# Kernel tuning notes

Measured on AMD Instinct MI355X. Metric: run time of the kernel, lower is better.

## Reference

```python
import jax, jax.numpy as jnp
import numpy as np

N_NODES = 100000
N_EDGES = 3200000


def gcn_conv(x, row, col, W, n):
    # PyG GCNConv: x @ W, then D^{-1/2}(A+I)D^{-1/2} aggregation (self-loops added).
    h = x @ W  # [N, out]
    loop = jnp.arange(n)
    r = jnp.concatenate([row, loop])
    c = jnp.concatenate([col, loop])
    deg = jax.ops.segment_sum(jnp.ones_like(c, dtype=h.dtype), c, num_segments=n)
    dinv = jnp.where(deg > 0, jax.lax.rsqrt(deg), 0.0)
    norm = dinv[r] * dinv[c]  # [E+N]
    msg = h[r] * norm[:, None]  # gather + scale
    return jax.ops.segment_sum(msg, c, num_segments=n)  # scatter-add


def setup_inputs() -> dict:
    key = jax.random.key(0)
    k1, k2, k3, k4, k5 = jax.random.split(key, 5)
    x = jax.random.normal(k1, (N_NODES, 1), dtype=jnp.float32)
    edge_index = jax.random.randint(k2, (2, N_EDGES), 0, N_NODES, dtype=jnp.int64)
    W1 = jax.random.normal(k3, (1, 16), dtype=jnp.float32) * 0.5
    W2 = jax.random.normal(k4, (16, 16), dtype=jnp.float32) * 0.25
    W3 = jax.random.normal(k5, (16, 11), dtype=jnp.float32) * 0.25
    b = jnp.zeros((11,), dtype=jnp.float32)
    return {"x": x, "edge_index": edge_index, "W1": W1, "W2": W2, "W3": W3, "b": b}


def reference(x, edge_index, W1, W2, W3, b):
    n = x.shape[0]
    row, col = edge_index[0], edge_index[1]
    h = jax.nn.relu(gcn_conv(x, row, col, W1, n))
    h = jax.nn.relu(gcn_conv(h, row, col, W2, n))
    g = jnp.mean(h, axis=0).reshape(-1, 16)  # [1,16] graph readout
    out = (g @ W3).squeeze() + b  # [11]
    return out
```

## Files before the change

kernel.cpp:

```cpp
#include <hip/hip_runtime.h>

static constexpr int N = 100000;
static constexpr int E = 3200000;
static constexpr int BUKSHIFT = 8;
static constexpr int BUKSZ = 1 << BUKSHIFT;
static constexpr int BUKMASK = BUKSZ - 1;
static constexpr int NBUK = (N + BUKSZ - 1) / BUKSZ;
static constexpr int CAP = 12288;
static constexpr int SC_CHUNK = 8192;
static constexpr int SC_T = 1024;
static constexpr int SC_BLOCKS = (E + SC_CHUNK - 1) / SC_CHUNK;


__global__ void k_init(int* __restrict__ gofs) {
    int i = threadIdx.x;
    if (i < NBUK) gofs[i] = i * CAP;
}

__global__ __launch_bounds__(SC_T) void k_scatter(const int4* __restrict__ rows4,
                                                  const int4* __restrict__ cols4,
                                                  int* __restrict__ gofs,
                                                  int* __restrict__ binned) {
    __shared__ int hist[4][NBUK];
    __shared__ int cnt[512];
    __shared__ int lbase[NBUK];
    __shared__ int gbase[NBUK];
    __shared__ int stag[SC_CHUNK];

    const int tid = threadIdx.x;
    const int g = tid >> 8;
    for (int i = tid; i < 4 * NBUK; i += SC_T) (&hist[0][0])[i] = 0;
    if (tid < 512) cnt[tid] = 0;
    __syncthreads();

    const int nI4 = E / 4;
    const int base4 = blockIdx.x * (SC_CHUNK / 4);
    const int ia = base4 + tid, ib = base4 + 1024 + tid;
    const bool va = ia < nI4, vb = ib < nI4;
    int4 ra, ca, rb, cb;
    if (va) { ra = rows4[ia]; ca = cols4[ia]; }
    if (vb) { rb = rows4[ib]; cb = cols4[ib]; }

    if (va) {
        atomicAdd(&hist[g][ca.x >> BUKSHIFT], 1);
        atomicAdd(&hist[g][ca.y >> BUKSHIFT], 1);
        atomicAdd(&hist[g][ca.z >> BUKSHIFT], 1);
        atomicAdd(&hist[g][ca.w >> BUKSHIFT], 1);
    }
    if (vb) {
        atomicAdd(&hist[g][cb.x >> BUKSHIFT], 1);
        atomicAdd(&hist[g][cb.y >> BUKSHIFT], 1);
        atomicAdd(&hist[g][cb.z >> BUKSHIFT], 1);
        atomicAdd(&hist[g][cb.w >> BUKSHIFT], 1);
    }
    __syncthreads();

    if (tid < NBUK) {
        int h0 = hist[0][tid], h1 = hist[1][tid], h2 = hist[2][tid], h3 = hist[3][tid];
        hist[0][tid] = 0; hist[1][tid] = h0; hist[2][tid] = h0 + h1; hist[3][tid] = h0 + h1 + h2;
        int c = h0 + h1 + h2 + h3;
        cnt[tid] = c;
        gbase[tid] = c ? atomicAdd(&gofs[tid], c) : 0;
    }
    __syncthreads();
    for (int off = 1; off < 512; off <<= 1) {
        int v = 0;
        if (tid < 512) { v = cnt[tid]; if (tid >= off) v += cnt[tid - off]; }
        __syncthreads();
        if (tid < 512) cnt[tid] = v;
        __syncthreads();
    }
    if (tid < NBUK) lbase[tid] = tid ? cnt[tid - 1] : 0;
    __syncthreads();

    if (va) {
        int b, off;
        b = ca.x >> BUKSHIFT; off = atomicAdd(&hist[g][b], 1); stag[lbase[b] + off] = (ra.x << BUKSHIFT) | (ca.x & BUKMASK);
        b = ca.y >> BUKSHIFT; off = atomicAdd(&hist[g][b], 1); stag[lbase[b] + off] = (ra.y << BUKSHIFT) | (ca.y & BUKMASK);
        b = ca.z >> BUKSHIFT; off = atomicAdd(&hist[g][b], 1); stag[lbase[b] + off] = (ra.z << BUKSHIFT) | (ca.z & BUKMASK);
        b = ca.w >> BUKSHIFT; off = atomicAdd(&hist[g][b], 1); stag[lbase[b] + off] = (ra.w << BUKSHIFT) | (ca.w & BUKMASK);
    }
    if (vb) {
        int b, off;
        b = cb.x >> BUKSHIFT; off = atomicAdd(&hist[g][b], 1); stag[lbase[b] + off] = (rb.x << BUKSHIFT) | (cb.x & BUKMASK);
        b = cb.y >> BUKSHIFT; off = atomicAdd(&hist[g][b], 1); stag[lbase[b] + off] = (rb.y << BUKSHIFT) | (cb.y & BUKMASK);
        b = cb.z >> BUKSHIFT; off = atomicAdd(&hist[g][b], 1); stag[lbase[b] + off] = (rb.z << BUKSHIFT) | (cb.z & BUKMASK);
        b = cb.w >> BUKSHIFT; off = atomicAdd(&hist[g][b], 1); stag[lbase[b] + off] = (rb.w << BUKSHIFT) | (cb.w & BUKMASK);
    }
    __syncthreads();

    const int eTot = min(SC_CHUNK, E - blockIdx.x * SC_CHUNK);
    int s = tid * 8;
    if (s < eTot) {
        int lo = 0, hi = NBUK - 1;
        while (lo < hi) { int mid = (lo + hi + 1) >> 1; if (lbase[mid] <= s) lo = mid; else hi = mid - 1; }
        int b = lo;
        const int e1 = min(s + 8, eTot);
        for (; s < e1; ++s) {
            while (b + 1 < NBUK && lbase[b + 1] <= s) ++b;
            binned[gbase[b] + (s - lbase[b])] = stag[s];
        }
    }
}

__global__ void k_deg(const int* __restrict__ binned, const int* __restrict__ gofs,
                      const float* __restrict__ x, float* __restrict__ dinv,
                      float* __restrict__ y1) {
    __shared__ int cnt[2][BUKSZ];
    const int tid = threadIdx.x;
    cnt[0][tid] = 0; cnt[1][tid] = 0;
    __syncthreads();
    const int b = blockIdx.x, g = tid >> 7;
    const int s1 = gofs[b];
    for (int i = b * CAP + tid; i < s1; i += 256)
        atomicAdd(&cnt[g][binned[i] & BUKMASK], 1);
    __syncthreads();
    const int v = (b << BUKSHIFT) + tid;
    if (v < N) {
        float d = rsqrtf(1.0f + (float)(cnt[0][tid] + cnt[1][tid]));
        dinv[v] = d;
        y1[v] = d * x[v];
    }
}

__global__ void k_acc1(const int* __restrict__ binned, const int* __restrict__ gofs,
                       const float* __restrict__ y1, const float* __restrict__ dinv,
                       float* __restrict__ m) {
    __shared__ float acc[2][BUKSZ];
    const int tid = threadIdx.x;
    acc[0][tid] = 0.f; acc[1][tid] = 0.f;
    __syncthreads();
    const int b = blockIdx.x, g = tid >> 7;
    const int s1 = gofs[b];
    for (int i = b * CAP + tid; i < s1; i += 256) {
        int p = binned[i];
        atomicAdd(&acc[g][p & BUKMASK], y1[p >> BUKSHIFT]);
    }
    __syncthreads();
    const int v = (b << BUKSHIFT) + tid;
    if (v < N) {
        float d = dinv[v];
        float s = d * (acc[0][tid] + acc[1][tid]) + d * y1[v];
        m[v] = d * s;
    }
}

__global__ void k_acc2(const int* __restrict__ binned, const int* __restrict__ gofs,
                       const float* __restrict__ m, const float* __restrict__ dinv,
                       const float* __restrict__ W1, const float* __restrict__ W2,
                       float* __restrict__ partials) {
    __shared__ float tp[2][BUKSZ], tn[2][BUKSZ];
    __shared__ float sP[16], sM[16], sAcc[16];
    const int tid = threadIdx.x;
    if (tid < 16) {
        float p = 0.f, q = 0.f;
        for (int k = 0; k < 16; ++k) {
            float w1 = W1[k];
            float w2 = W2[k * 16 + tid];
            p += fmaxf(w1, 0.f) * w2;
            q += fminf(w1, 0.f) * w2;
        }
        sP[tid] = p; sM[tid] = q; sAcc[tid] = 0.f;
    }
    tp[0][tid] = 0.f; tp[1][tid] = 0.f; tn[0][tid] = 0.f; tn[1][tid] = 0.f;
    __syncthreads();
    const int b = blockIdx.x, g = tid >> 7;
    const int s1 = gofs[b];
    for (int i = b * CAP + tid; i < s1; i += 256) {
        int p = binned[i];
        float val = m[p >> BUKSHIFT];
        atomicAdd(val >= 0.f ? &tp[g][p & BUKMASK] : &tn[g][p & BUKMASK], val);
    }
    __syncthreads();
    const int v = (b << BUKSHIFT) + tid;
    float alpha = 0.f, beta = 0.f;
    if (v < N) {
        float d = dinv[v], mv = m[v];
        alpha = d * (tp[0][tid] + tp[1][tid]);
        beta  = d * (tn[0][tid] + tn[1][tid]);
        float self = d * mv;
        if (mv >= 0.f) alpha += self; else beta += self;
    }
    const int lane = tid & 63;
    for (int j = 0; j < 16; ++j) {
        float h = fmaxf(alpha * sP[j] + beta * sM[j], 0.f);
        #pragma unroll
        for (int off = 32; off > 0; off >>= 1) h += __shfl_down(h, off);
        if (lane == 0) atomicAdd(&sAcc[j], h);
    }
    __syncthreads();
    if (tid < 16) partials[b * 16 + tid] = sAcc[tid];
}

__global__ void k_out(const float* __restrict__ partials, const float* __restrict__ W3,
                      const float* __restrict__ b, float* __restrict__ out) {
    __shared__ float s[16][16];
    int j = threadIdx.x & 15;
    int g = threadIdx.x >> 4;
    float acc = 0.f;
    for (int blk = g; blk < NBUK; blk += 16) acc += partials[blk * 16 + j];
    s[g][j] = acc;
    __syncthreads();
    if (threadIdx.x < 16) {
        float tot = 0.f;
        #pragma unroll
        for (int gg = 0; gg < 16; ++gg) tot += s[gg][threadIdx.x];
        s[0][threadIdx.x] = tot * (1.0f / (float)N);
    }
    __syncthreads();
    if (threadIdx.x < 11) {
        float acc2 = b[threadIdx.x];
        #pragma unroll
        for (int k = 0; k < 16; ++k) acc2 += s[0][k] * W3[k * 11 + threadIdx.x];
        out[threadIdx.x] = acc2;
    }
}

extern "C" void kernel_launch(void* const* d_in, const int* in_sizes, int n_in,
                              void* d_out, int out_size, void* d_ws, size_t ws_size,
                              hipStream_t stream) {
    const float* x  = (const float*)d_in[0];
    const int*   ei = (const int*)d_in[1];
    const float* W1 = (const float*)d_in[2];
    const float* W2 = (const float*)d_in[3];
    const float* W3 = (const float*)d_in[4];
    const float* b  = (const float*)d_in[5];
    float* out = (float*)d_out;

    int*   wsi      = (int*)d_ws;
    int*   binned   = wsi;
    float* dinv     = (float*)(wsi + (size_t)NBUK * CAP);
    float* y1       = dinv + N;
    float* m        = y1 + N;
    int*   gofs     = (int*)(m + N);
    float* partials = (float*)(gofs + NBUK);

    const int4* rows4 = (const int4*)ei;
    const int4* cols4 = (const int4*)(ei + E);

    k_init   <<<1, 512, 0, stream>>>(gofs);
    k_scatter<<<SC_BLOCKS, SC_T, 0, stream>>>(rows4, cols4, gofs, binned);
    k_deg    <<<NBUK, 256, 0, stream>>>(binned, gofs, x, dinv, y1);
    k_acc1   <<<NBUK, 256, 0, stream>>>(binned, gofs, y1, dinv, m);
    k_acc2   <<<NBUK, 256, 0, stream>>>(binned, gofs, m, dinv, W1, W2, partials);
    k_out    <<<1, 256, 0, stream>>>(partials, W3, b, out);
}
```

Before: 104.8 us.

## Widen bucket kernels to 1024 threads with int4 loads and larger scatter chunks

The degree and both aggregation kernels now run 1024 threads per bucket. Each kernel reads the binned edge list as int4 and spreads its shared-memory atomics over 8 privatized histogram copies, which are summed at the end. The scatter kernel now handles 16384 edges per block, with each thread loading four int4 vectors. The goal is more memory-level parallelism and less contention on shared-memory atomics. The cost is half as many scatter blocks, which may leave CUs idle, and a larger shared-memory footprint per block.

```diff
diff --git a/kernel.cpp b/kernel.cpp
--- a/kernel.cpp
+++ b/kernel.cpp
@@ -7,7 +7,7 @@
 static constexpr int BUKMASK = BUKSZ - 1;
 static constexpr int NBUK = (N + BUKSZ - 1) / BUKSZ;
 static constexpr int CAP = 12288;
-static constexpr int SC_CHUNK = 8192;
+static constexpr int SC_CHUNK = 16384;
 static constexpr int SC_T = 1024;
 static constexpr int SC_BLOCKS = (E + SC_CHUNK - 1) / SC_CHUNK;
 
@@ -35,32 +35,29 @@
 
     const int nI4 = E / 4;
     const int base4 = blockIdx.x * (SC_CHUNK / 4);
-    const int ia = base4 + tid, ib = base4 + 1024 + tid;
-    const bool va = ia < nI4, vb = ib < nI4;
-    int4 ra, ca, rb, cb;
-    if (va) { ra = rows4[ia]; ca = cols4[ia]; }
-    if (vb) { rb = rows4[ib]; cb = cols4[ib]; }
-
-    if (va) {
-        atomicAdd(&hist[g][ca.x >> BUKSHIFT], 1);
-        atomicAdd(&hist[g][ca.y >> BUKSHIFT], 1);
-        atomicAdd(&hist[g][ca.z >> BUKSHIFT], 1);
-        atomicAdd(&hist[g][ca.w >> BUKSHIFT], 1);
-    }
-    if (vb) {
-        atomicAdd(&hist[g][cb.x >> BUKSHIFT], 1);
-        atomicAdd(&hist[g][cb.y >> BUKSHIFT], 1);
-        atomicAdd(&hist[g][cb.z >> BUKSHIFT], 1);
-        atomicAdd(&hist[g][cb.w >> BUKSHIFT], 1);
+    int4 r[4], c[4];
+    bool vld[4];
+    #pragma unroll
+    for (int k = 0; k < 4; ++k) {
+        int idx = base4 + k * SC_T + tid;
+        vld[k] = idx < nI4;
+        if (vld[k]) { r[k] = rows4[idx]; c[k] = cols4[idx]; }
+    }
+    #pragma unroll
+    for (int k = 0; k < 4; ++k) if (vld[k]) {
+        atomicAdd(&hist[g][c[k].x >> BUKSHIFT], 1);
+        atomicAdd(&hist[g][c[k].y >> BUKSHIFT], 1);
+        atomicAdd(&hist[g][c[k].z >> BUKSHIFT], 1);
+        atomicAdd(&hist[g][c[k].w >> BUKSHIFT], 1);
     }
     __syncthreads();
 
     if (tid < NBUK) {
         int h0 = hist[0][tid], h1 = hist[1][tid], h2 = hist[2][tid], h3 = hist[3][tid];
         hist[0][tid] = 0; hist[1][tid] = h0; hist[2][tid] = h0 + h1; hist[3][tid] = h0 + h1 + h2;
-        int c = h0 + h1 + h2 + h3;
-        cnt[tid] = c;
-        gbase[tid] = c ? atomicAdd(&gofs[tid], c) : 0;
+        int cc = h0 + h1 + h2 + h3;
+        cnt[tid] = cc;
+        gbase[tid] = cc ? atomicAdd(&gofs[tid], cc) : 0;
     }
     __syncthreads();
     for (int off = 1; off < 512; off <<= 1) {
@@ -73,29 +70,23 @@
     if (tid < NBUK) lbase[tid] = tid ? cnt[tid - 1] : 0;
     __syncthreads();
 
-    if (va) {
+    #pragma unroll
+    for (int k = 0; k < 4; ++k) if (vld[k]) {
         int b, off;
-        b = ca.x >> BUKSHIFT; off = atomicAdd(&hist[g][b], 1); stag[lbase[b] + off] = (ra.x << BUKSHIFT) | (ca.x & BUKMASK);
-        b = ca.y >> BUKSHIFT; off = atomicAdd(&hist[g][b], 1); stag[lbase[b] + off] = (ra.y << BUKSHIFT) | (ca.y & BUKMASK);
-        b = ca.z >> BUKSHIFT; off = atomicAdd(&hist[g][b], 1); stag[lbase[b] + off] = (ra.z << BUKSHIFT) | (ca.z & BUKMASK);
-        b = ca.w >> BUKSHIFT; off = atomicAdd(&hist[g][b], 1); stag[lbase[b] + off] = (ra.w << BUKSHIFT) | (ca.w & BUKMASK);
-    }
-    if (vb) {
-        int b, off;
-        b = cb.x >> BUKSHIFT; off = atomicAdd(&hist[g][b], 1); stag[lbase[b] + off] = (rb.x << BUKSHIFT) | (cb.x & BUKMASK);
-        b = cb.y >> BUKSHIFT; off = atomicAdd(&hist[g][b], 1); stag[lbase[b] + off] = (rb.y << BUKSHIFT) | (cb.y & BUKMASK);
-        b = cb.z >> BUKSHIFT; off = atomicAdd(&hist[g][b], 1); stag[lbase[b] + off] = (rb.z << BUKSHIFT) | (cb.z & BUKMASK);
-        b = cb.w >> BUKSHIFT; off = atomicAdd(&hist[g][b], 1); stag[lbase[b] + off] = (rb.w << BUKSHIFT) | (cb.w & BUKMASK);
+        b = c[k].x >> BUKSHIFT; off = atomicAdd(&hist[g][b], 1); stag[lbase[b] + off] = (r[k].x << BUKSHIFT) | (c[k].x & BUKMASK);
+        b = c[k].y >> BUKSHIFT; off = atomicAdd(&hist[g][b], 1); stag[lbase[b] + off] = (r[k].y << BUKSHIFT) | (c[k].y & BUKMASK);
+        b = c[k].z >> BUKSHIFT; off = atomicAdd(&hist[g][b], 1); stag[lbase[b] + off] = (r[k].z << BUKSHIFT) | (c[k].z & BUKMASK);
+        b = c[k].w >> BUKSHIFT; off = atomicAdd(&hist[g][b], 1); stag[lbase[b] + off] = (r[k].w << BUKSHIFT) | (c[k].w & BUKMASK);
     }
     __syncthreads();
 
     const int eTot = min(SC_CHUNK, E - blockIdx.x * SC_CHUNK);
-    int s = tid * 8;
+    int s = tid * 16;
     if (s < eTot) {
         int lo = 0, hi = NBUK - 1;
         while (lo < hi) { int mid = (lo + hi + 1) >> 1; if (lbase[mid] <= s) lo = mid; else hi = mid - 1; }
         int b = lo;
-        const int e1 = min(s + 8, eTot);
+        const int e1 = min(s + 16, eTot);
         for (; s < e1; ++s) {
             while (b + 1 < NBUK && lbase[b + 1] <= s) ++b;
             binned[gbase[b] + (s - lbase[b])] = stag[s];
@@ -103,53 +94,89 @@
     }
 }
 
-__global__ void k_deg(const int* __restrict__ binned, const int* __restrict__ gofs,
-                      const float* __restrict__ x, float* __restrict__ dinv,
-                      float* __restrict__ y1) {
-    __shared__ int cnt[2][BUKSZ];
-    const int tid = threadIdx.x;
-    cnt[0][tid] = 0; cnt[1][tid] = 0;
+__global__ __launch_bounds__(1024) void k_deg(const int* __restrict__ binned,
+                                              const int* __restrict__ gofs,
+                                              const float* __restrict__ x,
+                                              float* __restrict__ dinv,
+                                              float* __restrict__ y1) {
+    __shared__ int cnt[8][BUKSZ];
+    const int tid = threadIdx.x;
+    for (int i = tid; i < 8 * BUKSZ; i += 1024) (&cnt[0][0])[i] = 0;
     __syncthreads();
     const int b = blockIdx.x, g = tid >> 7;
-    const int s1 = gofs[b];
-    for (int i = b * CAP + tid; i < s1; i += 256)
-        atomicAdd(&cnt[g][binned[i] & BUKMASK], 1);
-    __syncthreads();
-    const int v = (b << BUKSHIFT) + tid;
-    if (v < N) {
-        float d = rsqrtf(1.0f + (float)(cnt[0][tid] + cnt[1][tid]));
-        dinv[v] = d;
-        y1[v] = d * x[v];
-    }
-}
-
-__global__ void k_acc1(const int* __restrict__ binned, const int* __restrict__ gofs,
-                       const float* __restrict__ y1, const float* __restrict__ dinv,
-                       float* __restrict__ m) {
-    __shared__ float acc[2][BUKSZ];
-    const int tid = threadIdx.x;
-    acc[0][tid] = 0.f; acc[1][tid] = 0.f;
+    const int s0 = b * CAP;
+    const int n = gofs[b] - s0;
+    const int n4 = n >> 2;
+    const int4* b4 = (const int4*)(binned + s0);
+    for (int i = tid; i < n4; i += 1024) {
+        int4 p = b4[i];
+        atomicAdd(&cnt[g][p.x & BUKMASK], 1);
+        atomicAdd(&cnt[g][p.y & BUKMASK], 1);
+        atomicAdd(&cnt[g][p.z & BUKMASK], 1);
+        atomicAdd(&cnt[g][p.w & BUKMASK], 1);
+    }
+    if (tid < (n & 3)) atomicAdd(&cnt[g][binned[s0 + (n4 << 2) + tid] & BUKMASK], 1);
+    __syncthreads();
+    if (tid < BUKSZ) {
+        int v = (b << BUKSHIFT) + tid;
+        if (v < N) {
+            int c = 0;
+            #pragma unroll
+            for (int q = 0; q < 8; ++q) c += cnt[q][tid];
+            float d = rsqrtf(1.0f + (float)c);
+            dinv[v] = d;
+            y1[v] = d * x[v];
+        }
+    }
+}
+
+__global__ __launch_bounds__(1024) void k_acc1(const int* __restrict__ binned,
+                                               const int* __restrict__ gofs,
+                                               const float* __restrict__ y1,
+                                               const float* __restrict__ dinv,
+                                               float* __restrict__ m) {
+    __shared__ float acc[8][BUKSZ];
+    const int tid = threadIdx.x;
+    for (int i = tid; i < 8 * BUKSZ; i += 1024) (&acc[0][0])[i] = 0.f;
     __syncthreads();
     const int b = blockIdx.x, g = tid >> 7;
-    const int s1 = gofs[b];
-    for (int i = b * CAP + tid; i < s1; i += 256) {
-        int p = binned[i];
+    const int s0 = b * CAP;
+    const int n = gofs[b] - s0;
+    const int n4 = n >> 2;
+    const int4* b4 = (const int4*)(binned + s0);
+    for (int i = tid; i < n4; i += 1024) {
+        int4 p = b4[i];
+        atomicAdd(&acc[g][p.x & BUKMASK], y1[p.x >> BUKSHIFT]);
+        atomicAdd(&acc[g][p.y & BUKMASK], y1[p.y >> BUKSHIFT]);
+        atomicAdd(&acc[g][p.z & BUKMASK], y1[p.z >> BUKSHIFT]);
+        atomicAdd(&acc[g][p.w & BUKMASK], y1[p.w >> BUKSHIFT]);
+    }
+    if (tid < (n & 3)) {
+        int p = binned[s0 + (n4 << 2) + tid];
         atomicAdd(&acc[g][p & BUKMASK], y1[p >> BUKSHIFT]);
     }
     __syncthreads();
-    const int v = (b << BUKSHIFT) + tid;
-    if (v < N) {
-        float d = dinv[v];
-        float s = d * (acc[0][tid] + acc[1][tid]) + d * y1[v];
-        m[v] = d * s;
-    }
-}
-
-__global__ void k_acc2(const int* __restrict__ binned, const int* __restrict__ gofs,
-                       const float* __restrict__ m, const float* __restrict__ dinv,
-                       const float* __restrict__ W1, const float* __restrict__ W2,
-                       float* __restrict__ partials) {
-    __shared__ float tp[2][BUKSZ], tn[2][BUKSZ];
+    if (tid < BUKSZ) {
+        int v = (b << BUKSHIFT) + tid;
+        if (v < N) {
+            float a = 0.f;
+            #pragma unroll
+            for (int q = 0; q < 8; ++q) a += acc[q][tid];
+            float d = dinv[v];
+            float s = d * a + d * y1[v];
+            m[v] = d * s;
+        }
+    }
+}
+
+__global__ __launch_bounds__(1024) void k_acc2(const int* __restrict__ binned,
+                                               const int* __restrict__ gofs,
+                                               const float* __restrict__ m,
+                                               const float* __restrict__ dinv,
+                                               const float* __restrict__ W1,
+                                               const float* __restrict__ W2,
+                                               float* __restrict__ partials) {
+    __shared__ float tp[8][BUKSZ], tn[8][BUKSZ];
     __shared__ float sP[16], sM[16], sAcc[16];
     const int tid = threadIdx.x;
     if (tid < 16) {
@@ -162,31 +189,48 @@
         }
         sP[tid] = p; sM[tid] = q; sAcc[tid] = 0.f;
     }
-    tp[0][tid] = 0.f; tp[1][tid] = 0.f; tn[0][tid] = 0.f; tn[1][tid] = 0.f;
+    for (int i = tid; i < 8 * BUKSZ; i += 1024) { (&tp[0][0])[i] = 0.f; (&tn[0][0])[i] = 0.f; }
     __syncthreads();
     const int b = blockIdx.x, g = tid >> 7;
-    const int s1 = gofs[b];
-    for (int i = b * CAP + tid; i < s1; i += 256) {
-        int p = binned[i];
+    const int s0 = b * CAP;
+    const int n = gofs[b] - s0;
+    const int n4 = n >> 2;
+    const int4* b4 = (const int4*)(binned + s0);
+    for (int i = tid; i < n4; i += 1024) {
+        int4 p = b4[i];
+        float v0 = m[p.x >> BUKSHIFT], v1 = m[p.y >> BUKSHIFT];
+        float v2 = m[p.z >> BUKSHIFT], v3 = m[p.w >> BUKSHIFT];
+        atomicAdd(v0 >= 0.f ? &tp[g][p.x & BUKMASK] : &tn[g][p.x & BUKMASK], v0);
+        atomicAdd(v1 >= 0.f ? &tp[g][p.y & BUKMASK] : &tn[g][p.y & BUKMASK], v1);
+        atomicAdd(v2 >= 0.f ? &tp[g][p.z & BUKMASK] : &tn[g][p.z & BUKMASK], v2);
+        atomicAdd(v3 >= 0.f ? &tp[g][p.w & BUKMASK] : &tn[g][p.w & BUKMASK], v3);
+    }
+    if (tid < (n & 3)) {
+        int p = binned[s0 + (n4 << 2) + tid];
         float val = m[p >> BUKSHIFT];
         atomicAdd(val >= 0.f ? &tp[g][p & BUKMASK] : &tn[g][p & BUKMASK], val);
     }
     __syncthreads();
-    const int v = (b << BUKSHIFT) + tid;
     float alpha = 0.f, beta = 0.f;
-    if (v < N) {
-        float d = dinv[v], mv = m[v];
-        alpha = d * (tp[0][tid] + tp[1][tid]);
-        beta  = d * (tn[0][tid] + tn[1][tid]);
-        float self = d * mv;
-        if (mv >= 0.f) alpha += self; else beta += self;
+    if (tid < BUKSZ) {
+        int v = (b << BUKSHIFT) + tid;
+        if (v < N) {
+            float a = 0.f, bb = 0.f;
+            #pragma unroll
+            for (int q = 0; q < 8; ++q) { a += tp[q][tid]; bb += tn[q][tid]; }
+            float d = dinv[v], mv = m[v];
+            alpha = d * a;
+            beta  = d * bb;
+            float self = d * mv;
+            if (mv >= 0.f) alpha += self; else beta += self;
+        }
     }
     const int lane = tid & 63;
     for (int j = 0; j < 16; ++j) {
         float h = fmaxf(alpha * sP[j] + beta * sM[j], 0.f);
         #pragma unroll
         for (int off = 32; off > 0; off >>= 1) h += __shfl_down(h, off);
-        if (lane == 0) atomicAdd(&sAcc[j], h);
+        if (lane == 0 && h != 0.f) atomicAdd(&sAcc[j], h);
     }
     __syncthreads();
     if (tid < 16) partials[b * 16 + tid] = sAcc[tid];
@@ -240,8 +284,8 @@
 
     k_init   <<<1, 512, 0, stream>>>(gofs);
     k_scatter<<<SC_BLOCKS, SC_T, 0, stream>>>(rows4, cols4, gofs, binned);
-    k_deg    <<<NBUK, 256, 0, stream>>>(binned, gofs, x, dinv, y1);
-    k_acc1   <<<NBUK, 256, 0, stream>>>(binned, gofs, y1, dinv, m);
-    k_acc2   <<<NBUK, 256, 0, stream>>>(binned, gofs, m, dinv, W1, W2, partials);
+    k_deg    <<<NBUK, 1024, 0, stream>>>(binned, gofs, x, dinv, y1);
+    k_acc1   <<<NBUK, 1024, 0, stream>>>(binned, gofs, y1, dinv, m);
+    k_acc2   <<<NBUK, 1024, 0, stream>>>(binned, gofs, m, dinv, W1, W2, partials);
     k_out    <<<1, 256, 0, stream>>>(partials, W3, b, out);
 }
```

New measurement: 110.6 us. +5.6%, slower.
